# Kernel tuning notes

Measured on AMD Instinct MI355X. Metric: run time of the kernel, lower is better.

The kernel has to match this reference:

```python
import jax, jax.numpy as jnp
import numpy as np


def _grid_mesh(n):
    ys, xs = np.meshgrid(np.arange(n), np.arange(n), indexing='ij')
    verts = np.stack([xs, ys, np.zeros_like(xs)], -1).reshape(-1, 3).astype(np.float32) / (n - 1)
    idx = np.arange(n * n).reshape(n, n)
    v00 = idx[:-1, :-1].ravel(); v01 = idx[:-1, 1:].ravel()
    v10 = idx[1:, :-1].ravel(); v11 = idx[1:, 1:].ravel()
    faces = np.concatenate([np.stack([v00, v10, v01], 1), np.stack([v01, v10, v11], 1)], 0).astype(np.int32)
    e = np.concatenate([faces[:, [0, 1]], faces[:, [1, 2]], faces[:, [2, 0]]], 0)
    e = np.unique(np.sort(e, axis=1), axis=0).astype(np.int32)
    return verts, faces, e


def setup_inputs() -> dict:
    N_GRID, B, S = 200, 2, 5000
    verts_np, faces_np, edges_np = _grid_mesh(N_GRID)
    verts_np[:, 2] = 0.1 * np.sin(2 * np.pi * verts_np[:, 0]) * np.sin(2 * np.pi * verts_np[:, 1])
    key = jax.random.key(0)
    k1, k2, k3, k4 = jax.random.split(key, 4)
    verts_std = jnp.asarray(verts_np)
    verts_scr = verts_std[None] + 5e-4 * jax.random.normal(k1, (B,) + verts_std.shape, jnp.float32)
    xy = jax.random.uniform(k2, (B, S, 2), jnp.float32)
    z = 0.1 * jnp.sin(2 * jnp.pi * xy[..., 0]) * jnp.sin(2 * jnp.pi * xy[..., 1])
    trg_points = jnp.concatenate([xy, z[..., None]], -1)
    rand_face_u = jax.random.uniform(k3, (B, S), jnp.float32)
    rand_bary = jax.random.uniform(k4, (B, S, 2), jnp.float32)
    return {
        'verts_scr': verts_scr,
        'verts_std': verts_std,
        'trg_points': trg_points,
        'rand_face_u': rand_face_u,
        'rand_bary': rand_bary,
        'faces': jnp.asarray(faces_np),
        'edges': jnp.asarray(edges_np),
    }


def _cot_edges(verts, faces):
    # pytorch3d cot_laplacian: per-face cotangents, symmetrized edge list (6F entries).
    v0, v1, v2 = verts[faces[:, 0]], verts[faces[:, 1]], verts[faces[:, 2]]
    A = jnp.linalg.norm(v1 - v2, axis=1)
    B = jnp.linalg.norm(v0 - v2, axis=1)
    C = jnp.linalg.norm(v0 - v1, axis=1)
    A2, B2, C2 = A * A, B * B, C * C
    s = 0.5 * (A + B + C)
    area = jnp.sqrt(jnp.clip(s * (s - A) * (s - B) * (s - C), 1e-12, None))
    cot = jnp.stack([B2 + C2 - A2, A2 + C2 - B2, A2 + B2 - C2], axis=1) / (4.0 * area[:, None])
    ii = faces[:, jnp.array([1, 2, 0])].reshape(-1)
    jj = faces[:, jnp.array([2, 0, 1])].reshape(-1)
    src = jnp.concatenate([ii, jj])
    dst = jnp.concatenate([jj, ii])
    w = jnp.concatenate([cot.reshape(-1), cot.reshape(-1)])
    return src, dst, w


def _sample_points(verts, faces, u_face, r_bary):
    # area-weighted face sampling + pytorch3d barycentric coords
    v0, v1, v2 = verts[faces[:, 0]], verts[faces[:, 1]], verts[faces[:, 2]]
    areas = 0.5 * jnp.linalg.norm(jnp.cross(v1 - v0, v2 - v0), axis=1)
    cdf = jnp.cumsum(areas) / jnp.sum(areas)
    fidx = jnp.clip(jnp.searchsorted(cdf, u_face), 0, faces.shape[0] - 1)
    su = jnp.sqrt(r_bary[:, 0])
    w0, w1, w2 = 1.0 - su, su * (1.0 - r_bary[:, 1]), su * r_bary[:, 1]
    return w0[:, None] * v0[fidx] + w1[:, None] * v1[fidx] + w2[:, None] * v2[fidx]


def _chamfer(x, y):
    # squared-distance chamfer, mean over points then batch (pytorch3d defaults)
    d = (jnp.sum(x * x, -1)[:, :, None] + jnp.sum(y * y, -1)[:, None, :]
         - 2.0 * jnp.einsum('bsd,btd->bst', x, y))
    return jnp.min(d, 2).mean() + jnp.min(d, 1).mean()


def _forward(verts_scr, verts_std, trg_points, rand_face_u, rand_bary, faces, edges):
    Vn = verts_std.shape[0]
    # chamfer between sampled src surface points and target point cloud
    sample_scr = jax.vmap(lambda v, u, r: _sample_points(v, faces, u, r))(verts_scr, rand_face_u, rand_bary)
    loss_p0 = _chamfer(sample_scr, trg_points)
    loss_n1 = jnp.asarray(1e-5, verts_scr.dtype)  # tensor-target branch

    # cot laplacian smoothing (method='cot')
    def lap_one(v):
        src, dst, w = _cot_edges(v, faces)
        Lv = jax.ops.segment_sum(w[:, None] * v[dst], src, num_segments=Vn)
        rw = jax.ops.segment_sum(w, src, num_segments=Vn)
        inv = jnp.where(rw > 0, 1.0 / jnp.maximum(rw, 1e-12), 0.0)
        return jnp.linalg.norm(Lv * inv[:, None] - v, axis=1).mean()

    loss_lap = jax.vmap(lap_one)(verts_scr).mean()

    # edge loss against mean edge length of the std mesh
    target_len = jnp.linalg.norm(verts_std[edges[:, 0]] - verts_std[edges[:, 1]], axis=1).mean()
    elen = jnp.linalg.norm(verts_scr[:, edges[:, 0]] - verts_scr[:, edges[:, 1]], axis=-1)
    loss_edge = ((elen - target_len) ** 2).mean()

    # ARAP rigid loss on std-mesh cot connectivity/weights
    src, dst, w = _cot_edges(verts_std, faces)
    e_std = verts_std[src] - verts_std[dst]

    def rigid_one(v):
        e_scr = v[src] - v[dst]
        S = jax.ops.segment_sum(w[:, None, None] * e_std[:, :, None] * e_scr[:, None, :], src, num_segments=Vn)
        U, _, Vt = jnp.linalg.svd(S)
        R = jnp.matmul(jnp.swapaxes(Vt, -1, -2), jnp.swapaxes(U, -1, -2))
        flip = jnp.where(jnp.linalg.det(R) < 0, -1.0, 1.0)
        Vt2 = Vt.at[:, -1, :].multiply(flip[:, None])
        R = jnp.matmul(jnp.swapaxes(Vt2, -1, -2), jnp.swapaxes(U, -1, -2))
        res = e_scr - jnp.einsum('eij,ej->ei', R[src], e_std)
        return jax.ops.segment_sum(w * jnp.sum(res * res, 1), src, num_segments=Vn)

    loss_rigid = jax.vmap(rigid_one)(verts_scr).mean()
    return jnp.stack([loss_p0, loss_n1, loss_lap, loss_edge, loss_rigid])


def reference(verts_scr, verts_std, trg_points, rand_face_u, rand_bary, faces, edges):
    return _forward(verts_scr, verts_std, trg_points, rand_face_u, rand_bary, faces, edges)
```

## Files before the change

### kernel.cpp

```cpp
#include <hip/hip_runtime.h>
#include <math.h>

#define TPB 256
#define MAXDEG 8

static __device__ __forceinline__ void atomAddD(double* p, double v) {
  __hip_atomic_fetch_add(p, v, __ATOMIC_RELAXED, __HIP_MEMORY_SCOPE_AGENT);
}

static __device__ __forceinline__ double bredsum(double v) {
  __shared__ double sb[TPB];
  int t = threadIdx.x;
  sb[t] = v;
  __syncthreads();
  for (int o = TPB / 2; o > 0; o >>= 1) {
    if (t < o) sb[t] += sb[t + o];
    __syncthreads();
  }
  double r = sb[0];
  __syncthreads();
  return r;
}

template <int p, int q, int r>
static __device__ __forceinline__ void jrot(double A[3][3], double V[3][3]) {
  double apq = A[p][q];
  if (apq == 0.0) return;
  double app = A[p][p], aqq = A[q][q];
  double theta = (aqq - app) / (2.0 * apq);
  double t = 1.0 / (fabs(theta) + sqrt(theta * theta + 1.0));
  if (theta < 0.0) t = -t;
  double c = 1.0 / sqrt(t * t + 1.0), sn = t * c;
  A[p][p] = app - t * apq;
  A[q][q] = aqq + t * apq;
  A[p][q] = 0.0;
  A[q][p] = 0.0;
  double arp = A[r][p], arq = A[r][q];
  A[r][p] = c * arp - sn * arq; A[p][r] = A[r][p];
  A[r][q] = sn * arp + c * arq; A[q][r] = A[r][q];
#pragma unroll
  for (int k = 0; k < 3; k++) {
    double vkp = V[k][p], vkq = V[k][q];
    V[k][p] = c * vkp - sn * vkq;
    V[k][q] = sn * vkp + c * vkq;
  }
}

#define ESWAP(la, lax, lay, laz, lb, lbx, lby, lbz)                       \
  if (la < lb) {                                                          \
    double t_;                                                            \
    t_ = la; la = lb; lb = t_;                                            \
    t_ = lax; lax = lbx; lbx = t_;                                        \
    t_ = lay; lay = lby; lby = t_;                                        \
    t_ = laz; laz = lbz; lbz = t_;                                        \
  }

static __device__ void kabschR(const double S[3][3], double R9[9]) {
  double A[3][3];
#pragma unroll
  for (int a = 0; a < 3; a++)
#pragma unroll
    for (int c = 0; c < 3; c++)
      A[a][c] = S[0][a] * S[0][c] + S[1][a] * S[1][c] + S[2][a] * S[2][c];
  double V[3][3] = {{1, 0, 0}, {0, 1, 0}, {0, 0, 1}};
  for (int sw = 0; sw < 12; sw++) {
    double off = fabs(A[0][1]) + fabs(A[0][2]) + fabs(A[1][2]);
    double dia = fabs(A[0][0]) + fabs(A[1][1]) + fabs(A[2][2]);
    if (!(off > dia * 1e-15)) break;
    jrot<0, 1, 2>(A, V);
    jrot<0, 2, 1>(A, V);
    jrot<1, 2, 0>(A, V);
  }
  double l0 = A[0][0], l1 = A[1][1], l2 = A[2][2];
  double a0x = V[0][0], a0y = V[1][0], a0z = V[2][0];
  double a1x = V[0][1], a1y = V[1][1], a1z = V[2][1];
  double a2x = V[0][2], a2y = V[1][2], a2z = V[2][2];
  ESWAP(l0, a0x, a0y, a0z, l1, a1x, a1y, a1z);
  ESWAP(l0, a0x, a0y, a0z, l2, a2x, a2y, a2z);
  ESWAP(l1, a1x, a1y, a1z, l2, a2x, a2y, a2z);
  double R00 = 1, R01 = 0, R02 = 0, R10 = 0, R11 = 1, R12 = 0, R20 = 0, R21 = 0, R22 = 1;
  double b1x = S[0][0] * a0x + S[0][1] * a0y + S[0][2] * a0z;
  double b1y = S[1][0] * a0x + S[1][1] * a0y + S[1][2] * a0z;
  double b1z = S[2][0] * a0x + S[2][1] * a0y + S[2][2] * a0z;
  double b2x = S[0][0] * a1x + S[0][1] * a1y + S[0][2] * a1z;
  double b2y = S[1][0] * a1x + S[1][1] * a1y + S[1][2] * a1z;
  double b2z = S[2][0] * a1x + S[2][1] * a1y + S[2][2] * a1z;
  double n1 = sqrt(b1x * b1x + b1y * b1y + b1z * b1z);
  if (n1 > 1e-300 && isfinite(n1)) {
    double u1x = b1x / n1, u1y = b1y / n1, u1z = b1z / n1;
    double dp = u1x * b2x + u1y * b2y + u1z * b2z;
    b2x -= dp * u1x; b2y -= dp * u1y; b2z -= dp * u1z;
    double n2 = sqrt(b2x * b2x + b2y * b2y + b2z * b2z);
    double u2x, u2y, u2z;
    if (n2 > n1 * 1e-14) {
      u2x = b2x / n2; u2y = b2y / n2; u2z = b2z / n2;
    } else {
      double f0 = fabs(u1x), f1 = fabs(u1y), f2 = fabs(u1z);
      double e0, e1, e2;
      if (f0 <= f1 && f0 <= f2) { e0 = 1.0 - u1x * u1x; e1 = -u1x * u1y; e2 = -u1x * u1z; }
      else if (f1 <= f2)        { e0 = -u1y * u1x; e1 = 1.0 - u1y * u1y; e2 = -u1y * u1z; }
      else                      { e0 = -u1z * u1x; e1 = -u1z * u1y; e2 = 1.0 - u1z * u1z; }
      double nw = sqrt(e0 * e0 + e1 * e1 + e2 * e2);
      u2x = e0 / nw; u2y = e1 / nw; u2z = e2 / nw;
    }
    double u3x = u1y * u2z - u1z * u2y;
    double u3y = u1z * u2x - u1x * u2z;
    double u3z = u1x * u2y - u1y * u2x;
    double w3x = a0y * a1z - a0z * a1y;
    double w3y = a0z * a1x - a0x * a1z;
    double w3z = a0x * a1y - a0y * a1x;
    R00 = a0x * u1x + a1x * u2x + w3x * u3x;
    R01 = a0x * u1y + a1x * u2y + w3x * u3y;
    R02 = a0x * u1z + a1x * u2z + w3x * u3z;
    R10 = a0y * u1x + a1y * u2x + w3y * u3x;
    R11 = a0y * u1y + a1y * u2y + w3y * u3y;
    R12 = a0y * u1z + a1y * u2z + w3y * u3z;
    R20 = a0z * u1x + a1z * u2x + w3z * u3x;
    R21 = a0z * u1y + a1z * u2y + w3z * u3y;
    R22 = a0z * u1z + a1z * u2z + w3z * u3z;
  }
  R9[0] = R00; R9[1] = R01; R9[2] = R02;
  R9[3] = R10; R9[4] = R11; R9[5] = R12;
  R9[6] = R20; R9[7] = R21; R9[8] = R22;
}

static __device__ __forceinline__ void heronCots(double A2, double B2, double C2,
                                                 double* c0, double* c1, double* c2) {
  double A = sqrt(A2), Bl = sqrt(B2), C = sqrt(C2);
  double s = 0.5 * (A + Bl + C);
  double pr = s * (s - A) * (s - Bl) * (s - C);
  pr = pr < 1e-12 ? 1e-12 : pr;
  double inv4 = 1.0 / (4.0 * sqrt(pr));
  *c0 = (B2 + C2 - A2) * inv4;
  *c1 = (A2 + C2 - B2) * inv4;
  *c2 = (A2 + B2 - C2) * inv4;
}

__global__ void kPrep(const float* vscr, const float* vstd, const int* faces,
                      const int* edges, double* cdf, double* ccot, double* scot,
                      int* adjcnt, int4* adjtab, double* accEdgeStd,
                      int B, int Vn, int F, int E) {
  int i = blockIdx.x * TPB + threadIdx.x;
  if (i < B * F) {
    int b = i / F, f = i % F;
    const float* vb = vscr + (size_t)b * Vn * 3;
    int i0 = faces[f * 3], i1 = faces[f * 3 + 1], i2 = faces[f * 3 + 2];
    {
      double p0x = vb[i0 * 3], p0y = vb[i0 * 3 + 1], p0z = vb[i0 * 3 + 2];
      double p1x = vb[i1 * 3], p1y = vb[i1 * 3 + 1], p1z = vb[i1 * 3 + 2];
      double p2x = vb[i2 * 3], p2y = vb[i2 * 3 + 1], p2z = vb[i2 * 3 + 2];
      double ax = p1x - p0x, ay = p1y - p0y, az = p1z - p0z;
      double bx = p2x - p0x, by = p2y - p0y, bz = p2z - p0z;
      double cx = ay * bz - az * by, cy = az * bx - ax * bz, cz = ax * by - ay * bx;
      cdf[i] = 0.5 * sqrt(cx * cx + cy * cy + cz * cz);
      double dx = p1x - p2x, dy = p1y - p2y, dz = p1z - p2z;
      double A2 = dx * dx + dy * dy + dz * dz;
      double B2 = bx * bx + by * by + bz * bz;
      double C2 = ax * ax + ay * ay + az * az;
      double c0, c1, c2;
      heronCots(A2, B2, C2, &c0, &c1, &c2);
      ccot[(size_t)i * 3 + 0] = c0;
      ccot[(size_t)i * 3 + 1] = c1;
      ccot[(size_t)i * 3 + 2] = c2;
    }
    if (b == 0) {
      double p0x = vstd[i0 * 3], p0y = vstd[i0 * 3 + 1], p0z = vstd[i0 * 3 + 2];
      double p1x = vstd[i1 * 3], p1y = vstd[i1 * 3 + 1], p1z = vstd[i1 * 3 + 2];
      double p2x = vstd[i2 * 3], p2y = vstd[i2 * 3 + 1], p2z = vstd[i2 * 3 + 2];
      double ax = p1x - p0x, ay = p1y - p0y, az = p1z - p0z;
      double bx = p2x - p0x, by = p2y - p0y, bz = p2z - p0z;
      double dx = p1x - p2x, dy = p1y - p2y, dz = p1z - p2z;
      double A2 = dx * dx + dy * dy + dz * dz;
      double B2 = bx * bx + by * by + bz * bz;
      double C2 = ax * ax + ay * ay + az * az;
      double c0, c1, c2;
      heronCots(A2, B2, C2, &c0, &c1, &c2);
      scot[(size_t)f * 3 + 0] = c0;
      scot[(size_t)f * 3 + 1] = c1;
      scot[(size_t)f * 3 + 2] = c2;
      int f3 = f * 3;
      int s0 = atomicAdd(&adjcnt[i0], 1);
      if (s0 < MAXDEG) adjtab[(size_t)i0 * MAXDEG + s0] = make_int4(i1, i2, f3 + 1, f3 + 2);
      int s1 = atomicAdd(&adjcnt[i1], 1);
      if (s1 < MAXDEG) adjtab[(size_t)i1 * MAXDEG + s1] = make_int4(i2, i0, f3 + 2, f3 + 0);
      int s2 = atomicAdd(&adjcnt[i2], 1);
      if (s2 < MAXDEG) adjtab[(size_t)i2 * MAXDEG + s2] = make_int4(i0, i1, f3 + 0, f3 + 1);
    }
  }
  double eval = 0.0;
  if (i < E) {
    int e0 = edges[(size_t)i * 2], e1 = edges[(size_t)i * 2 + 1];
    double dx = (double)vstd[e0 * 3 + 0] - vstd[e1 * 3 + 0];
    double dy = (double)vstd[e0 * 3 + 1] - vstd[e1 * 3 + 1];
    double dz = (double)vstd[e0 * 3 + 2] - vstd[e1 * 3 + 2];
    eval = sqrt(dx * dx + dy * dy + dz * dz);
  }
  double r = bredsum(eval);
  if (threadIdx.x == 0) atomAddD(accEdgeStd, r);
}

__global__ void kScanFused(double* a, double* bsum, double* boffs, int F, int nc,
                           int B, int* cnt) {
  int blk = blockIdx.x;
  int b = blk / nc, c = blk % nc;
  int t = threadIdx.x, lane = t & 63, wid = t >> 6;
  int f = c * 1024 + t;
  size_t idx = (size_t)b * F + f;
  double v = (f < F) ? a[idx] : 0.0;
  double x = v;
#pragma unroll
  for (int o = 1; o < 64; o <<= 1) {
    double y = __shfl_up(x, o, 64);
    if (lane >= o) x += y;
  }
  __shared__ double wsum[16];
  __shared__ double woffs[16];
  if (lane == 63) wsum[wid] = x;
  __syncthreads();
  if (wid == 0) {
    double s = (lane < 16) ? wsum[lane] : 0.0;
    double xs = s;
#pragma unroll
    for (int o = 1; o < 16; o <<= 1) {
      double y = __shfl_up(xs, o, 64);
      if (lane >= o) xs += y;
    }
    double ex = __shfl_up(xs, 1, 64);
    if (lane < 16) woffs[lane] = (lane == 0) ? 0.0 : ex;
  }
  __syncthreads();
  x += woffs[wid];
  if (f < F) a[idx] = x;
  if (t == 1023) bsum[(size_t)b * nc + c] = x;
  __syncthreads();
  __shared__ int amlast;
  if (t == 0) {
    __threadfence();
    int old = __hip_atomic_fetch_add(cnt, 1, __ATOMIC_ACQ_REL, __HIP_MEMORY_SCOPE_AGENT);
    amlast = (old == (int)gridDim.x - 1) ? 1 : 0;
  }
  __syncthreads();
  if (amlast && wid == 0) {
    for (int bb = 0; bb < B; bb++) {
      double carry = 0.0;
      for (int base = 0; base < nc; base += 64) {
        int cc = base + lane;
        double s = (cc < nc) ? bsum[(size_t)bb * nc + cc] : 0.0;
        double xs = s;
#pragma unroll
        for (int o = 1; o < 64; o <<= 1) {
          double y = __shfl_up(xs, o, 64);
          if (lane >= o) xs += y;
        }
        double ex = __shfl_up(xs, 1, 64);
        double excl = (lane == 0) ? 0.0 : ex;
        if (cc < nc) boffs[(size_t)bb * nc + cc] = carry + excl;
        carry += __shfl(xs, 63, 64);
      }
    }
  }
}

__global__ void kSample(const float* verts, const int* faces, const double* cdf,
                        const double* bsum, const double* boffs,
                        const float* rfu, const float* rbary, float* samples,
                        int B, int Vn, int F, int S, int nc) {
  int i = blockIdx.x * blockDim.x + threadIdx.x;
  if (i >= B * S) return;
  int b = i / S;
  const double* bo = boffs + (size_t)b * nc;
  const double* bs = bsum + (size_t)b * nc;
  double total = bo[nc - 1] + bs[nc - 1];
  double tgt = (double)rfu[i] * total;
  int lo = 0, hi = nc;
  while (lo < hi) {
    int m = (lo + hi) >> 1;
    if (bo[m] + bs[m] < tgt) lo = m + 1; else hi = m;
  }
  int c = lo < nc ? lo : nc - 1;
  double thr = tgt - bo[c];
  const double* cc = cdf + (size_t)b * F + (size_t)c * 1024;
  int lim = F - c * 1024; if (lim > 1024) lim = 1024;
  lo = 0; hi = lim;
  while (lo < hi) {
    int m = (lo + hi) >> 1;
    if (cc[m] < thr) lo = m + 1; else hi = m;
  }
  int j = lo < lim ? lo : lim - 1;
  int f = c * 1024 + j;
  const float* vb = verts + (size_t)b * Vn * 3;
  int i0 = faces[f * 3], i1 = faces[f * 3 + 1], i2 = faces[f * 3 + 2];
  float r0 = rbary[(size_t)i * 2], r1 = rbary[(size_t)i * 2 + 1];
  float su = sqrtf(r0);
  float w0 = 1.f - su, w1 = su * (1.f - r1), w2 = su * r1;
  samples[(size_t)i * 3 + 0] = w0 * vb[i0 * 3 + 0] + w1 * vb[i1 * 3 + 0] + w2 * vb[i2 * 3 + 0];
  samples[(size_t)i * 3 + 1] = w0 * vb[i0 * 3 + 1] + w1 * vb[i1 * 3 + 1] + w2 * vb[i2 * 3 + 1];
  samples[(size_t)i * 3 + 2] = w0 * vb[i0 * 3 + 2] + w1 * vb[i1 * 3 + 2] + w2 * vb[i2 * 3 + 2];
}

__global__ void kChamferBoth(const float* smp, const float* trg, unsigned* rowmin,
                             int B, int S) {
  int z = blockIdx.z;
  int dir = z / B, b = z % B;
  const float* X = dir ? trg : smp;
  const float* Y = dir ? smp : trg;
  int i = blockIdx.x * TPB + threadIdx.x;
  int j0 = blockIdx.y * TPB;
  int n = min(TPB, S - j0);
  __shared__ float4 sy[TPB];
  const float* Yb = Y + ((size_t)b * S + j0) * 3;
  if ((int)threadIdx.x < n) {
    int t = threadIdx.x;
    sy[t] = make_float4(Yb[t * 3], Yb[t * 3 + 1], Yb[t * 3 + 2], 0.f);
  }
  __syncthreads();
  if (i >= S) return;
  const float* Xb = X + (size_t)b * S * 3;
  float x0 = Xb[i * 3], x1 = Xb[i * 3 + 1], x2 = Xb[i * 3 + 2];
  float inf = __int_as_float(0x7f800000);
  float m0 = inf, m1 = inf, m2 = inf, m3 = inf;
  int k = 0;
  for (; k + 4 <= n; k += 4) {
    float4 y0 = sy[k], y1 = sy[k + 1], y2 = sy[k + 2], y3 = sy[k + 3];
    float a0 = x0 - y0.x, b0 = x1 - y0.y, c0 = x2 - y0.z;
    float a1 = x0 - y1.x, b1 = x1 - y1.y, c1 = x2 - y1.z;
    float a2 = x0 - y2.x, b2 = x1 - y2.y, c2 = x2 - y2.z;
    float a3 = x0 - y3.x, b3 = x1 - y3.y, c3 = x2 - y3.z;
    m0 = fminf(m0, a0 * a0 + b0 * b0 + c0 * c0);
    m1 = fminf(m1, a1 * a1 + b1 * b1 + c1 * c1);
    m2 = fminf(m2, a2 * a2 + b2 * b2 + c2 * c2);
    m3 = fminf(m3, a3 * a3 + b3 * b3 + c3 * c3);
  }
  for (; k < n; k++) {
    float4 y = sy[k];
    float a = x0 - y.x, bb = x1 - y.y, cc = x2 - y.z;
    m0 = fminf(m0, a * a + bb * bb + cc * cc);
  }
  float mn = fminf(fminf(m0, m1), fminf(m2, m3));
  atomicMin(&rowmin[((size_t)dir * B + b) * S + i], __float_as_uint(mn));
}

__global__ void kMisc(const unsigned* rm, int nrm, const float* vscr, const int* edges,
                      int B, int Vn, int E, const double* tacc,
                      double* accCh, double* accEd) {
  int i = blockIdx.x * TPB + threadIdx.x;
  double v = 0.0;
  if (i < nrm) v = (double)__uint_as_float(rm[i]);
  double r = bredsum(v);
  if (threadIdx.x == 0) atomAddD(accCh, r);
  double tl = tacc[0] / (double)E;
  double val = 0.0;
  if (i < B * E) {
    int b = i / E, e = i % E;
    const float* vb = vscr + (size_t)b * Vn * 3;
    int e0 = edges[(size_t)e * 2], e1 = edges[(size_t)e * 2 + 1];
    double dx = (double)vb[e0 * 3 + 0] - vb[e1 * 3 + 0];
    double dy = (double)vb[e0 * 3 + 1] - vb[e1 * 3 + 1];
    double dz = (double)vb[e0 * 3 + 2] - vb[e1 * 3 + 2];
    double l = sqrt(dx * dx + dy * dy + dz * dz);
    double d = l - tl;
    val = d * d;
  }
  double r2 = bredsum(val);
  if (threadIdx.x == 0) atomAddD(accEd, r2);
}

__global__ void kVertexFin(const float* vstd, const float* vscr,
                           const int* cnt, const int4* adjtab, const double* scot,
                           const double* ccot, int B, int Vn, int F,
                           double* accum, int* done, float* out, int S, int E) {
  int idx = blockIdx.x * TPB + threadIdx.x;
  double vlap = 0.0, vrig = 0.0;
  if (idx < B * Vn) {
    int b = idx / Vn, v = idx % Vn;
    const float* cb = vscr + (size_t)b * Vn * 3;
    const double* ccb = ccot + (size_t)b * F * 3;
    double pasx = vstd[v * 3], pasy = vstd[v * 3 + 1], pasz = vstd[v * 3 + 2];
    double pacx = cb[v * 3], pacy = cb[v * 3 + 1], pacz = cb[v * 3 + 2];
    int n = cnt[v];
    if (n > MAXDEG) n = MAXDEG;
    const int4* at = adjtab + (size_t)v * MAXDEG;
    double S00 = 0, S01 = 0, S02 = 0, S10 = 0, S11 = 0, S12 = 0, S20 = 0, S21 = 0, S22 = 0;
    double Lx = 0, Ly = 0, Lz = 0, rw = 0, Qs = 0, Qc = 0;
    for (int k = 0; k < n; k++) {
      int4 e = at[k];
      int jb = e.x, jc = e.y;
      double cBs = scot[e.z], cCs = scot[e.w];
      double cBc = ccb[e.z], cCc = ccb[e.w];
      double pbsx = vstd[jb * 3], pbsy = vstd[jb * 3 + 1], pbsz = vstd[jb * 3 + 2];
      double pcsx = vstd[jc * 3], pcsy = vstd[jc * 3 + 1], pcsz = vstd[jc * 3 + 2];
      double pbcx = cb[jb * 3], pbcy = cb[jb * 3 + 1], pbcz = cb[jb * 3 + 2];
      double pccx = cb[jc * 3], pccy = cb[jc * 3 + 1], pccz = cb[jc * 3 + 2];
      Lx += cCc * pbcx + cBc * pccx;
      Ly += cCc * pbcy + cBc * pccy;
      Lz += cCc * pbcz + cBc * pccz;
      rw += cBc + cCc;
      double e1sx = pasx - pbsx, e1sy = pasy - pbsy, e1sz = pasz - pbsz;
      double e2sx = pasx - pcsx, e2sy = pasy - pcsy, e2sz = pasz - pcsz;
      double e1cx = pacx - pbcx, e1cy = pacy - pbcy, e1cz = pacz - pbcz;
      double e2cx = pacx - pccx, e2cy = pacy - pccy, e2cz = pacz - pccz;
      S00 += cCs * e1sx * e1cx + cBs * e2sx * e2cx;
      S01 += cCs * e1sx * e1cy + cBs * e2sx * e2cy;
      S02 += cCs * e1sx * e1cz + cBs * e2sx * e2cz;
      S10 += cCs * e1sy * e1cx + cBs * e2sy * e2cx;
      S11 += cCs * e1sy * e1cy + cBs * e2sy * e2cy;
      S12 += cCs * e1sy * e1cz + cBs * e2sy * e2cz;
      S20 += cCs * e1sz * e1cx + cBs * e2sz * e2cx;
      S21 += cCs * e1sz * e1cy + cBs * e2sz * e2cy;
      S22 += cCs * e1sz * e1cz + cBs * e2sz * e2cz;
      Qs += cCs * (e1sx * e1sx + e1sy * e1sy + e1sz * e1sz)
          + cBs * (e2sx * e2sx + e2sy * e2sy + e2sz * e2sz);
      Qc += cCs * (e1cx * e1cx + e1cy * e1cy + e1cz * e1cz)
          + cBs * (e2cx * e2cx + e2cy * e2cy + e2cz * e2cz);
    }
    double inv = (rw > 0.0) ? 1.0 / fmax(rw, 1e-12) : 0.0;
    double dx = Lx * inv - pacx, dy = Ly * inv - pacy, dz = Lz * inv - pacz;
    vlap = sqrt(dx * dx + dy * dy + dz * dz);
    double S[3][3] = {{S00, S01, S02}, {S10, S11, S12}, {S20, S21, S22}};
    double R9[9];
    kabschR(S, R9);
    double trRS = R9[0] * S00 + R9[1] * S10 + R9[2] * S20
                + R9[3] * S01 + R9[4] * S11 + R9[5] * S21
                + R9[6] * S02 + R9[7] * S12 + R9[8] * S22;
    vrig = Qc + Qs - 2.0 * trRS;
  }
  double r1 = bredsum(vlap);
  if (threadIdx.x == 0) atomAddD(accum + 1, r1);
  double r2 = bredsum(vrig);
  if (threadIdx.x == 0) atomAddD(accum + 4, r2);
  __shared__ int amlast;
  if (threadIdx.x == 0) {
    __threadfence();
    int old = __hip_atomic_fetch_add(done, 1, __ATOMIC_ACQ_REL, __HIP_MEMORY_SCOPE_AGENT);
    amlast = (old == (int)gridDim.x - 1) ? 1 : 0;
  }
  __syncthreads();
  if (amlast && threadIdx.x == 0) {
    double a0 = __hip_atomic_load(accum + 0, __ATOMIC_RELAXED, __HIP_MEMORY_SCOPE_AGENT);
    double a1 = __hip_atomic_load(accum + 1, __ATOMIC_RELAXED, __HIP_MEMORY_SCOPE_AGENT);
    double a3 = __hip_atomic_load(accum + 3, __ATOMIC_RELAXED, __HIP_MEMORY_SCOPE_AGENT);
    double a4 = __hip_atomic_load(accum + 4, __ATOMIC_RELAXED, __HIP_MEMORY_SCOPE_AGENT);
    out[0] = (float)(a0 / ((double)B * S));
    out[1] = 1e-5f;
    out[2] = (float)(a1 / ((double)B * Vn));
    out[3] = (float)(a3 / ((double)B * E));
    out[4] = (float)(a4 / ((double)B * Vn));
  }
}

extern "C" void kernel_launch(void* const* d_in, const int* in_sizes, int n_in,
                              void* d_out, int out_size, void* d_ws, size_t ws_size,
                              hipStream_t stream) {
  const float* vscr = (const float*)d_in[0];
  const float* vstd = (const float*)d_in[1];
  const float* trg  = (const float*)d_in[2];
  const float* rfu  = (const float*)d_in[3];
  const float* rby  = (const float*)d_in[4];
  const int* faces  = (const int*)d_in[5];
  const int* edges  = (const int*)d_in[6];
  float* out = (float*)d_out;

  int nVs = in_sizes[1];
  int Vn = nVs / 3;
  int B = in_sizes[0] / nVs;
  int S = in_sizes[3] / B;
  int F = in_sizes[5] / 3;
  int E = in_sizes[6] / 2;
  int nc = (F + 1023) / 1024;

  char* p = (char*)d_ws;
  auto alloc = [&](size_t bytes) -> void* {
    void* r = (void*)p;
    p += (bytes + 255) & ~(size_t)255;
    return r;
  };
  double* cdf   = (double*)alloc((size_t)B * F * sizeof(double));
  double* bsum  = (double*)alloc((size_t)B * nc * sizeof(double));
  double* boffs = (double*)alloc((size_t)B * nc * sizeof(double));
  double* scot  = (double*)alloc((size_t)F * 3 * sizeof(double));
  double* ccot  = (double*)alloc((size_t)B * F * 3 * sizeof(double));
  float* samples   = (float*)alloc((size_t)B * S * 3 * sizeof(float));
  unsigned* rowmin = (unsigned*)alloc((size_t)2 * B * S * sizeof(unsigned));
  int4* adjtab  = (int4*)alloc((size_t)Vn * MAXDEG * sizeof(int4));
  size_t zbytes = (size_t)Vn * sizeof(int) + 8 * sizeof(int) + 8 * sizeof(double);
  char* zbase   = (char*)alloc(zbytes);
  int* adjcnt   = (int*)zbase;
  int* cnts     = (int*)(zbase + (size_t)Vn * sizeof(int));
  double* accum = (double*)(zbase + (size_t)Vn * sizeof(int) + 8 * sizeof(int));

  hipMemsetAsync(zbase, 0, zbytes, stream);
  int nrm = 2 * B * S;
  hipMemsetAsync(rowmin, 0xFF, (size_t)nrm * sizeof(unsigned), stream);

  int BF = B * F;
  kPrep<<<(BF + TPB - 1) / TPB, TPB, 0, stream>>>(vscr, vstd, faces, edges, cdf, ccot,
                                                  scot, adjcnt, adjtab, accum + 2,
                                                  B, Vn, F, E);
  kScanFused<<<B * nc, 1024, 0, stream>>>(cdf, bsum, boffs, F, nc, B, cnts + 0);
  kSample<<<(B * S + TPB - 1) / TPB, TPB, 0, stream>>>(vscr, faces, cdf, bsum, boffs,
                                                       rfu, rby, samples, B, Vn, F, S, nc);
  dim3 cg((S + TPB - 1) / TPB, (S + TPB - 1) / TPB, 2 * B);
  kChamferBoth<<<cg, TPB, 0, stream>>>(samples, trg, rowmin, B, S);
  int nmisc = nrm > B * E ? nrm : B * E;
  kMisc<<<(nmisc + TPB - 1) / TPB, TPB, 0, stream>>>(rowmin, nrm, vscr, edges, B, Vn, E,
                                                     accum + 2, accum + 0, accum + 3);
  kVertexFin<<<(B * Vn + TPB - 1) / TPB, TPB, 0, stream>>>(vstd, vscr, adjcnt, adjtab,
                                                           scot, ccot, B, Vn, F,
                                                           accum, cnts + 1, out, S, E);
}
```

Baseline: 197.4 us.

## Fuse misc reductions into vertex kernel, double chamfer rows per thread, cap Jacobi sweeps

Removes the separate kMisc launch by folding the chamfer row-min sum and edge-length loss into kVertexFin, whose grid is enlarged to cover all three index ranges. The chamfer kernel now processes two query points per thread, so each shared-memory load of a target point is reused twice and half as many blocks are launched. The Jacobi eigen-solver sweep cap drops from 12 to 8. Edge threads in the fused kernel far outnumber vertex threads, so many blocks do light work alongside the heavy Kabsch blocks, and the lower sweep cap could cut convergence short for hard matrices.

```diff
diff --git a/kernel.cpp b/kernel.cpp
--- a/kernel.cpp
+++ b/kernel.cpp
@@ -63,7 +63,7 @@
     for (int c = 0; c < 3; c++)
       A[a][c] = S[0][a] * S[0][c] + S[1][a] * S[1][c] + S[2][a] * S[2][c];
   double V[3][3] = {{1, 0, 0}, {0, 1, 0}, {0, 0, 1}};
-  for (int sw = 0; sw < 12; sw++) {
+  for (int sw = 0; sw < 8; sw++) {
     double off = fabs(A[0][1]) + fabs(A[0][2]) + fabs(A[1][2]);
     double dia = fabs(A[0][0]) + fabs(A[1][1]) + fabs(A[2][2]);
     if (!(off > dia * 1e-15)) break;
@@ -304,7 +304,8 @@
   int dir = z / B, b = z % B;
   const float* X = dir ? trg : smp;
   const float* Y = dir ? smp : trg;
-  int i = blockIdx.x * TPB + threadIdx.x;
+  int ia = blockIdx.x * (TPB * 2) + threadIdx.x;
+  int ib = ia + TPB;
   int j0 = blockIdx.y * TPB;
   int n = min(TPB, S - j0);
   __shared__ float4 sy[TPB];
@@ -314,44 +315,47 @@
     sy[t] = make_float4(Yb[t * 3], Yb[t * 3 + 1], Yb[t * 3 + 2], 0.f);
   }
   __syncthreads();
-  if (i >= S) return;
   const float* Xb = X + (size_t)b * S * 3;
-  float x0 = Xb[i * 3], x1 = Xb[i * 3 + 1], x2 = Xb[i * 3 + 2];
+  bool aok = ia < S, bok = ib < S;
+  float ax = 0, ay = 0, az = 0, bx = 0, by = 0, bz = 0;
+  if (aok) { ax = Xb[ia * 3]; ay = Xb[ia * 3 + 1]; az = Xb[ia * 3 + 2]; }
+  if (bok) { bx = Xb[ib * 3]; by = Xb[ib * 3 + 1]; bz = Xb[ib * 3 + 2]; }
   float inf = __int_as_float(0x7f800000);
-  float m0 = inf, m1 = inf, m2 = inf, m3 = inf;
+  float ma0 = inf, ma1 = inf, mb0 = inf, mb1 = inf;
   int k = 0;
-  for (; k + 4 <= n; k += 4) {
-    float4 y0 = sy[k], y1 = sy[k + 1], y2 = sy[k + 2], y3 = sy[k + 3];
-    float a0 = x0 - y0.x, b0 = x1 - y0.y, c0 = x2 - y0.z;
-    float a1 = x0 - y1.x, b1 = x1 - y1.y, c1 = x2 - y1.z;
-    float a2 = x0 - y2.x, b2 = x1 - y2.y, c2 = x2 - y2.z;
-    float a3 = x0 - y3.x, b3 = x1 - y3.y, c3 = x2 - y3.z;
-    m0 = fminf(m0, a0 * a0 + b0 * b0 + c0 * c0);
-    m1 = fminf(m1, a1 * a1 + b1 * b1 + c1 * c1);
-    m2 = fminf(m2, a2 * a2 + b2 * b2 + c2 * c2);
-    m3 = fminf(m3, a3 * a3 + b3 * b3 + c3 * c3);
+  for (; k + 2 <= n; k += 2) {
+    float4 y0 = sy[k], y1 = sy[k + 1];
+    float a0 = ax - y0.x, a1 = ay - y0.y, a2 = az - y0.z;
+    float a3 = ax - y1.x, a4 = ay - y1.y, a5 = az - y1.z;
+    float b0 = bx - y0.x, b1 = by - y0.y, b2 = bz - y0.z;
+    float b3 = bx - y1.x, b4 = by - y1.y, b5 = bz - y1.z;
+    ma0 = fminf(ma0, a0 * a0 + a1 * a1 + a2 * a2);
+    ma1 = fminf(ma1, a3 * a3 + a4 * a4 + a5 * a5);
+    mb0 = fminf(mb0, b0 * b0 + b1 * b1 + b2 * b2);
+    mb1 = fminf(mb1, b3 * b3 + b4 * b4 + b5 * b5);
   }
   for (; k < n; k++) {
     float4 y = sy[k];
-    float a = x0 - y.x, bb = x1 - y.y, cc = x2 - y.z;
-    m0 = fminf(m0, a * a + bb * bb + cc * cc);
-  }
-  float mn = fminf(fminf(m0, m1), fminf(m2, m3));
-  atomicMin(&rowmin[((size_t)dir * B + b) * S + i], __float_as_uint(mn));
-}
-
-__global__ void kMisc(const unsigned* rm, int nrm, const float* vscr, const int* edges,
-                      int B, int Vn, int E, const double* tacc,
-                      double* accCh, double* accEd) {
-  int i = blockIdx.x * TPB + threadIdx.x;
-  double v = 0.0;
-  if (i < nrm) v = (double)__uint_as_float(rm[i]);
-  double r = bredsum(v);
-  if (threadIdx.x == 0) atomAddD(accCh, r);
-  double tl = tacc[0] / (double)E;
-  double val = 0.0;
-  if (i < B * E) {
-    int b = i / E, e = i % E;
+    float a0 = ax - y.x, a1 = ay - y.y, a2 = az - y.z;
+    float b0 = bx - y.x, b1 = by - y.y, b2 = bz - y.z;
+    ma0 = fminf(ma0, a0 * a0 + a1 * a1 + a2 * a2);
+    mb0 = fminf(mb0, b0 * b0 + b1 * b1 + b2 * b2);
+  }
+  size_t base = ((size_t)dir * B + b) * S;
+  if (aok) atomicMin(&rowmin[base + ia], __float_as_uint(fminf(ma0, ma1)));
+  if (bok) atomicMin(&rowmin[base + ib], __float_as_uint(fminf(mb0, mb1)));
+}
+
+__global__ void kVertexFin(const float* vstd, const float* vscr,
+                           const int* cnt, const int4* adjtab, const double* scot,
+                           const double* ccot, const unsigned* rm, int nrm,
+                           const int* edges, int B, int Vn, int F, int E,
+                           double* accum, int* done, float* out, int S) {
+  int idx = blockIdx.x * TPB + threadIdx.x;
+  double tl = accum[2] / (double)E;
+  double vedge = 0.0;
+  if (idx < B * E) {
+    int b = idx / E, e = idx % E;
     const float* vb = vscr + (size_t)b * Vn * 3;
     int e0 = edges[(size_t)e * 2], e1 = edges[(size_t)e * 2 + 1];
     double dx = (double)vb[e0 * 3 + 0] - vb[e1 * 3 + 0];
@@ -359,17 +363,10 @@
     double dz = (double)vb[e0 * 3 + 2] - vb[e1 * 3 + 2];
     double l = sqrt(dx * dx + dy * dy + dz * dz);
     double d = l - tl;
-    val = d * d;
-  }
-  double r2 = bredsum(val);
-  if (threadIdx.x == 0) atomAddD(accEd, r2);
-}
-
-__global__ void kVertexFin(const float* vstd, const float* vscr,
-                           const int* cnt, const int4* adjtab, const double* scot,
-                           const double* ccot, int B, int Vn, int F,
-                           double* accum, int* done, float* out, int S, int E) {
-  int idx = blockIdx.x * TPB + threadIdx.x;
+    vedge = d * d;
+  }
+  double vch = 0.0;
+  if (idx < nrm) vch = (double)__uint_as_float(rm[idx]);
   double vlap = 0.0, vrig = 0.0;
   if (idx < B * Vn) {
     int b = idx / Vn, v = idx % Vn;
@@ -424,10 +421,15 @@
                 + R9[6] * S02 + R9[7] * S12 + R9[8] * S22;
     vrig = Qc + Qs - 2.0 * trRS;
   }
-  double r1 = bredsum(vlap);
-  if (threadIdx.x == 0) atomAddD(accum + 1, r1);
-  double r2 = bredsum(vrig);
-  if (threadIdx.x == 0) atomAddD(accum + 4, r2);
+  double r;
+  r = bredsum(vedge);
+  if (threadIdx.x == 0) atomAddD(accum + 3, r);
+  r = bredsum(vch);
+  if (threadIdx.x == 0) atomAddD(accum + 0, r);
+  r = bredsum(vlap);
+  if (threadIdx.x == 0) atomAddD(accum + 1, r);
+  r = bredsum(vrig);
+  if (threadIdx.x == 0) atomAddD(accum + 4, r);
   __shared__ int amlast;
   if (threadIdx.x == 0) {
     __threadfence();
@@ -499,12 +501,13 @@
   kScanFused<<<B * nc, 1024, 0, stream>>>(cdf, bsum, boffs, F, nc, B, cnts + 0);
   kSample<<<(B * S + TPB - 1) / TPB, TPB, 0, stream>>>(vscr, faces, cdf, bsum, boffs,
                                                        rfu, rby, samples, B, Vn, F, S, nc);
-  dim3 cg((S + TPB - 1) / TPB, (S + TPB - 1) / TPB, 2 * B);
+  dim3 cg((S + TPB * 2 - 1) / (TPB * 2), (S + TPB - 1) / TPB, 2 * B);
   kChamferBoth<<<cg, TPB, 0, stream>>>(samples, trg, rowmin, B, S);
-  int nmisc = nrm > B * E ? nrm : B * E;
-  kMisc<<<(nmisc + TPB - 1) / TPB, TPB, 0, stream>>>(rowmin, nrm, vscr, edges, B, Vn, E,
-                                                     accum + 2, accum + 0, accum + 3);
-  kVertexFin<<<(B * Vn + TPB - 1) / TPB, TPB, 0, stream>>>(vstd, vscr, adjcnt, adjtab,
-                                                           scot, ccot, B, Vn, F,
-                                                           accum, cnts + 1, out, S, E);
-}
+  int nfin = B * E;
+  if (nfin < B * Vn) nfin = B * Vn;
+  if (nfin < nrm) nfin = nrm;
+  kVertexFin<<<(nfin + TPB - 1) / TPB, TPB, 0, stream>>>(vstd, vscr, adjcnt, adjtab,
+                                                         scot, ccot, rowmin, nrm, edges,
+                                                         B, Vn, F, E, accum, cnts + 1,
+                                                         out, S);
+}
```

Result: slower. 209.8 us (+6.3%).

## Split vertex finalize into 8-lane neighbor gather and separate Kabsch kernel

Applied to the files above, without the earlier changes.

The per-vertex loop over up to eight adjacency entries is spread across eight lanes, one neighbor each, and reduced with shuffles, so the gather loads run in parallel instead of serially per thread. The 3x3 covariance and the Q terms are written to a workspace buffer, and a second kernel runs the Jacobi-based Kabsch rotation one vertex per thread. The Jacobi sweep cap also drops from 12 to 8. This adds a kernel launch and a global round-trip of eleven doubles per vertex, and the lower sweep cap could cost accuracy on poorly conditioned matrices.

```diff
diff --git a/kernel.cpp b/kernel.cpp
--- a/kernel.cpp
+++ b/kernel.cpp
@@ -63,7 +63,7 @@
     for (int c = 0; c < 3; c++)
       A[a][c] = S[0][a] * S[0][c] + S[1][a] * S[1][c] + S[2][a] * S[2][c];
   double V[3][3] = {{1, 0, 0}, {0, 1, 0}, {0, 0, 1}};
-  for (int sw = 0; sw < 12; sw++) {
+  for (int sw = 0; sw < 8; sw++) {
     double off = fabs(A[0][1]) + fabs(A[0][2]) + fabs(A[1][2]);
     double dia = fabs(A[0][0]) + fabs(A[1][1]) + fabs(A[2][2]);
     if (!(off > dia * 1e-15)) break;
@@ -365,69 +365,107 @@
   if (threadIdx.x == 0) atomAddD(accEd, r2);
 }
 
-__global__ void kVertexFin(const float* vstd, const float* vscr,
-                           const int* cnt, const int4* adjtab, const double* scot,
-                           const double* ccot, int B, int Vn, int F,
-                           double* accum, int* done, float* out, int S, int E) {
-  int idx = blockIdx.x * TPB + threadIdx.x;
-  double vlap = 0.0, vrig = 0.0;
-  if (idx < B * Vn) {
-    int b = idx / Vn, v = idx % Vn;
+#define RED8(x) { x += __shfl_xor(x, 1, 8); x += __shfl_xor(x, 2, 8); x += __shfl_xor(x, 4, 8); }
+__global__ void kGather(const float* vstd, const float* vscr,
+                        const int* cnt, const int4* adjtab, const double* scot,
+                        const double* ccot, double* Sbuf, int B, int Vn, int F,
+                        double* accLap) {
+  int t = blockIdx.x * TPB + threadIdx.x;
+  int g = t >> 3, sub = t & 7;
+  int NG = B * Vn;
+  double vlap = 0.0;
+  if (g < NG) {
+    int b = g / Vn, v = g % Vn;
     const float* cb = vscr + (size_t)b * Vn * 3;
     const double* ccb = ccot + (size_t)b * F * 3;
     double pasx = vstd[v * 3], pasy = vstd[v * 3 + 1], pasz = vstd[v * 3 + 2];
     double pacx = cb[v * 3], pacy = cb[v * 3 + 1], pacz = cb[v * 3 + 2];
     int n = cnt[v];
     if (n > MAXDEG) n = MAXDEG;
-    const int4* at = adjtab + (size_t)v * MAXDEG;
-    double S00 = 0, S01 = 0, S02 = 0, S10 = 0, S11 = 0, S12 = 0, S20 = 0, S21 = 0, S22 = 0;
-    double Lx = 0, Ly = 0, Lz = 0, rw = 0, Qs = 0, Qc = 0;
-    for (int k = 0; k < n; k++) {
-      int4 e = at[k];
-      int jb = e.x, jc = e.y;
-      double cBs = scot[e.z], cCs = scot[e.w];
-      double cBc = ccb[e.z], cCc = ccb[e.w];
-      double pbsx = vstd[jb * 3], pbsy = vstd[jb * 3 + 1], pbsz = vstd[jb * 3 + 2];
-      double pcsx = vstd[jc * 3], pcsy = vstd[jc * 3 + 1], pcsz = vstd[jc * 3 + 2];
-      double pbcx = cb[jb * 3], pbcy = cb[jb * 3 + 1], pbcz = cb[jb * 3 + 2];
-      double pccx = cb[jc * 3], pccy = cb[jc * 3 + 1], pccz = cb[jc * 3 + 2];
-      Lx += cCc * pbcx + cBc * pccx;
-      Ly += cCc * pbcy + cBc * pccy;
-      Lz += cCc * pbcz + cBc * pccz;
-      rw += cBc + cCc;
-      double e1sx = pasx - pbsx, e1sy = pasy - pbsy, e1sz = pasz - pbsz;
-      double e2sx = pasx - pcsx, e2sy = pasy - pcsy, e2sz = pasz - pcsz;
-      double e1cx = pacx - pbcx, e1cy = pacy - pbcy, e1cz = pacz - pbcz;
-      double e2cx = pacx - pccx, e2cy = pacy - pccy, e2cz = pacz - pccz;
-      S00 += cCs * e1sx * e1cx + cBs * e2sx * e2cx;
-      S01 += cCs * e1sx * e1cy + cBs * e2sx * e2cy;
-      S02 += cCs * e1sx * e1cz + cBs * e2sx * e2cz;
-      S10 += cCs * e1sy * e1cx + cBs * e2sy * e2cx;
-      S11 += cCs * e1sy * e1cy + cBs * e2sy * e2cy;
-      S12 += cCs * e1sy * e1cz + cBs * e2sy * e2cz;
-      S20 += cCs * e1sz * e1cx + cBs * e2sz * e2cx;
-      S21 += cCs * e1sz * e1cy + cBs * e2sz * e2cy;
-      S22 += cCs * e1sz * e1cz + cBs * e2sz * e2cz;
-      Qs += cCs * (e1sx * e1sx + e1sy * e1sy + e1sz * e1sz)
-          + cBs * (e2sx * e2sx + e2sy * e2sy + e2sz * e2sz);
-      Qc += cCs * (e1cx * e1cx + e1cy * e1cy + e1cz * e1cz)
-          + cBs * (e2cx * e2cx + e2cy * e2cy + e2cz * e2cz);
+    int slot = sub < n ? sub : n - 1;
+    double m = (sub < n) ? 1.0 : 0.0;
+    int4 e = adjtab[(size_t)v * MAXDEG + slot];
+    int jb = e.x, jc = e.y;
+    double cBs = m * scot[e.z], cCs = m * scot[e.w];
+    double cBc = m * ccb[e.z], cCc = m * ccb[e.w];
+    double pbsx = vstd[jb * 3], pbsy = vstd[jb * 3 + 1], pbsz = vstd[jb * 3 + 2];
+    double pcsx = vstd[jc * 3], pcsy = vstd[jc * 3 + 1], pcsz = vstd[jc * 3 + 2];
+    double pbcx = cb[jb * 3], pbcy = cb[jb * 3 + 1], pbcz = cb[jb * 3 + 2];
+    double pccx = cb[jc * 3], pccy = cb[jc * 3 + 1], pccz = cb[jc * 3 + 2];
+    double Lx = cCc * pbcx + cBc * pccx;
+    double Ly = cCc * pbcy + cBc * pccy;
+    double Lz = cCc * pbcz + cBc * pccz;
+    double rw = cBc + cCc;
+    double e1sx = pasx - pbsx, e1sy = pasy - pbsy, e1sz = pasz - pbsz;
+    double e2sx = pasx - pcsx, e2sy = pasy - pcsy, e2sz = pasz - pcsz;
+    double e1cx = pacx - pbcx, e1cy = pacy - pbcy, e1cz = pacz - pbcz;
+    double e2cx = pacx - pccx, e2cy = pacy - pccy, e2cz = pacz - pccz;
+    double S00 = cCs * e1sx * e1cx + cBs * e2sx * e2cx;
+    double S01 = cCs * e1sx * e1cy + cBs * e2sx * e2cy;
+    double S02 = cCs * e1sx * e1cz + cBs * e2sx * e2cz;
+    double S10 = cCs * e1sy * e1cx + cBs * e2sy * e2cx;
+    double S11 = cCs * e1sy * e1cy + cBs * e2sy * e2cy;
+    double S12 = cCs * e1sy * e1cz + cBs * e2sy * e2cz;
+    double S20 = cCs * e1sz * e1cx + cBs * e2sz * e2cx;
+    double S21 = cCs * e1sz * e1cy + cBs * e2sz * e2cy;
+    double S22 = cCs * e1sz * e1cz + cBs * e2sz * e2cz;
+    double Qs = cCs * (e1sx * e1sx + e1sy * e1sy + e1sz * e1sz)
+              + cBs * (e2sx * e2sx + e2sy * e2sy + e2sz * e2sz);
+    double Qc = cCs * (e1cx * e1cx + e1cy * e1cy + e1cz * e1cz)
+              + cBs * (e2cx * e2cx + e2cy * e2cy + e2cz * e2cz);
+    RED8(S00) RED8(S01) RED8(S02)
+    RED8(S10) RED8(S11) RED8(S12)
+    RED8(S20) RED8(S21) RED8(S22)
+    RED8(Lx) RED8(Ly) RED8(Lz)
+    RED8(rw) RED8(Qs) RED8(Qc)
+    if (sub == 0) {
+      double inv = (rw > 0.0) ? 1.0 / fmax(rw, 1e-12) : 0.0;
+      double dx = Lx * inv - pacx, dy = Ly * inv - pacy, dz = Lz * inv - pacz;
+      vlap = sqrt(dx * dx + dy * dy + dz * dz);
+      Sbuf[(size_t)0 * NG + g] = S00;
+      Sbuf[(size_t)1 * NG + g] = S01;
+      Sbuf[(size_t)2 * NG + g] = S02;
+      Sbuf[(size_t)3 * NG + g] = S10;
+      Sbuf[(size_t)4 * NG + g] = S11;
+      Sbuf[(size_t)5 * NG + g] = S12;
+      Sbuf[(size_t)6 * NG + g] = S20;
+      Sbuf[(size_t)7 * NG + g] = S21;
+      Sbuf[(size_t)8 * NG + g] = S22;
+      Sbuf[(size_t)9 * NG + g] = Qs;
+      Sbuf[(size_t)10 * NG + g] = Qc;
     }
-    double inv = (rw > 0.0) ? 1.0 / fmax(rw, 1e-12) : 0.0;
-    double dx = Lx * inv - pacx, dy = Ly * inv - pacy, dz = Lz * inv - pacz;
-    vlap = sqrt(dx * dx + dy * dy + dz * dz);
-    double S[3][3] = {{S00, S01, S02}, {S10, S11, S12}, {S20, S21, S22}};
+  }
+  double r = bredsum(vlap);
+  if (threadIdx.x == 0) atomAddD(accLap, r);
+}
+
+__global__ void kKabschFin(const double* Sbuf, int B, int Vn,
+                           double* accum, int* done, float* out, int S, int E) {
+  int idx = blockIdx.x * TPB + threadIdx.x;
+  int NG = B * Vn;
+  double vrig = 0.0;
+  if (idx < NG) {
+    double S00 = Sbuf[(size_t)0 * NG + idx];
+    double S01 = Sbuf[(size_t)1 * NG + idx];
+    double S02 = Sbuf[(size_t)2 * NG + idx];
+    double S10 = Sbuf[(size_t)3 * NG + idx];
+    double S11 = Sbuf[(size_t)4 * NG + idx];
+    double S12 = Sbuf[(size_t)5 * NG + idx];
+    double S20 = Sbuf[(size_t)6 * NG + idx];
+    double S21 = Sbuf[(size_t)7 * NG + idx];
+    double S22 = Sbuf[(size_t)8 * NG + idx];
+    double Qs = Sbuf[(size_t)9 * NG + idx];
+    double Qc = Sbuf[(size_t)10 * NG + idx];
+    double Smat[3][3] = {{S00, S01, S02}, {S10, S11, S12}, {S20, S21, S22}};
     double R9[9];
-    kabschR(S, R9);
+    kabschR(Smat, R9);
     double trRS = R9[0] * S00 + R9[1] * S10 + R9[2] * S20
                 + R9[3] * S01 + R9[4] * S11 + R9[5] * S21
                 + R9[6] * S02 + R9[7] * S12 + R9[8] * S22;
     vrig = Qc + Qs - 2.0 * trRS;
   }
-  double r1 = bredsum(vlap);
-  if (threadIdx.x == 0) atomAddD(accum + 1, r1);
-  double r2 = bredsum(vrig);
-  if (threadIdx.x == 0) atomAddD(accum + 4, r2);
+  double r = bredsum(vrig);
+  if (threadIdx.x == 0) atomAddD(accum + 4, r);
   __shared__ int amlast;
   if (threadIdx.x == 0) {
     __threadfence();
@@ -479,6 +517,7 @@
   double* boffs = (double*)alloc((size_t)B * nc * sizeof(double));
   double* scot  = (double*)alloc((size_t)F * 3 * sizeof(double));
   double* ccot  = (double*)alloc((size_t)B * F * 3 * sizeof(double));
+  double* Sbuf  = (double*)alloc((size_t)11 * B * Vn * sizeof(double));
   float* samples   = (float*)alloc((size_t)B * S * 3 * sizeof(float));
   unsigned* rowmin = (unsigned*)alloc((size_t)2 * B * S * sizeof(unsigned));
   int4* adjtab  = (int4*)alloc((size_t)Vn * MAXDEG * sizeof(int4));
@@ -504,7 +543,10 @@
   int nmisc = nrm > B * E ? nrm : B * E;
   kMisc<<<(nmisc + TPB - 1) / TPB, TPB, 0, stream>>>(rowmin, nrm, vscr, edges, B, Vn, E,
                                                      accum + 2, accum + 0, accum + 3);
-  kVertexFin<<<(B * Vn + TPB - 1) / TPB, TPB, 0, stream>>>(vstd, vscr, adjcnt, adjtab,
-                                                           scot, ccot, B, Vn, F,
-                                                           accum, cnts + 1, out, S, E);
-}
+  int ngt = B * Vn * 8;
+  kGather<<<(ngt + TPB - 1) / TPB, TPB, 0, stream>>>(vstd, vscr, adjcnt, adjtab,
+                                                     scot, ccot, Sbuf, B, Vn, F,
+                                                     accum + 1);
+  kKabschFin<<<(B * Vn + TPB - 1) / TPB, TPB, 0, stream>>>(Sbuf, B, Vn, accum,
+                                                           cnts + 1, out, S, E);
+}
```

Result: slower. 229.2 us (+16.1%).

## Split per-vertex ARAP accumulation across four lanes and fold rowmin init into prep

Applied to the files above, without the earlier changes.

The vertex finalization kernel now gives each vertex four threads. Each thread handles up to two adjacency slots, and the partial sums are combined with width-4 shuffles, so the serial neighbor loop gets more parallelism. The rowmin initialization memset is replaced by writes inside kPrep, which removes a separate memset operation. The Jacobi sweep cap in the Kabsch solve drops from 12 to 8, which may reduce accuracy for slowly converging matrices. Having only one lane in four run the SVD leaves lanes idle, and the vertex kernel now launches four times as many threads.

```diff
diff --git a/kernel.cpp b/kernel.cpp
--- a/kernel.cpp
+++ b/kernel.cpp
@@ -63,7 +63,7 @@
     for (int c = 0; c < 3; c++)
       A[a][c] = S[0][a] * S[0][c] + S[1][a] * S[1][c] + S[2][a] * S[2][c];
   double V[3][3] = {{1, 0, 0}, {0, 1, 0}, {0, 0, 1}};
-  for (int sw = 0; sw < 12; sw++) {
+  for (int sw = 0; sw < 8; sw++) {
     double off = fabs(A[0][1]) + fabs(A[0][2]) + fabs(A[1][2]);
     double dia = fabs(A[0][0]) + fabs(A[1][1]) + fabs(A[2][2]);
     if (!(off > dia * 1e-15)) break;
@@ -139,8 +139,9 @@
 __global__ void kPrep(const float* vscr, const float* vstd, const int* faces,
                       const int* edges, double* cdf, double* ccot, double* scot,
                       int* adjcnt, int4* adjtab, double* accEdgeStd,
-                      int B, int Vn, int F, int E) {
+                      unsigned* rowmin, int nrm, int B, int Vn, int F, int E) {
   int i = blockIdx.x * TPB + threadIdx.x;
+  if (i < nrm) rowmin[i] = 0xFFFFFFFFu;
   if (i < B * F) {
     int b = i / F, f = i % F;
     const float* vb = vscr + (size_t)b * Vn * 3;
@@ -365,28 +366,33 @@
   if (threadIdx.x == 0) atomAddD(accEd, r2);
 }
 
+#define RED4(x) { x += __shfl_xor(x, 1, 4); x += __shfl_xor(x, 2, 4); }
 __global__ void kVertexFin(const float* vstd, const float* vscr,
                            const int* cnt, const int4* adjtab, const double* scot,
                            const double* ccot, int B, int Vn, int F,
                            double* accum, int* done, float* out, int S, int E) {
-  int idx = blockIdx.x * TPB + threadIdx.x;
+  int t = blockIdx.x * TPB + threadIdx.x;
+  int g = t >> 2, sub = t & 3;
   double vlap = 0.0, vrig = 0.0;
-  if (idx < B * Vn) {
-    int b = idx / Vn, v = idx % Vn;
+  if (g < B * Vn) {
+    int b = g / Vn, v = g % Vn;
     const float* cb = vscr + (size_t)b * Vn * 3;
     const double* ccb = ccot + (size_t)b * F * 3;
     double pasx = vstd[v * 3], pasy = vstd[v * 3 + 1], pasz = vstd[v * 3 + 2];
     double pacx = cb[v * 3], pacy = cb[v * 3 + 1], pacz = cb[v * 3 + 2];
     int n = cnt[v];
     if (n > MAXDEG) n = MAXDEG;
-    const int4* at = adjtab + (size_t)v * MAXDEG;
     double S00 = 0, S01 = 0, S02 = 0, S10 = 0, S11 = 0, S12 = 0, S20 = 0, S21 = 0, S22 = 0;
     double Lx = 0, Ly = 0, Lz = 0, rw = 0, Qs = 0, Qc = 0;
-    for (int k = 0; k < n; k++) {
-      int4 e = at[k];
+#pragma unroll
+    for (int k = 0; k < 2; k++) {
+      int slot = sub + 4 * k;
+      int sl = slot < n ? slot : n - 1;
+      double m = (slot < n) ? 1.0 : 0.0;
+      int4 e = adjtab[(size_t)v * MAXDEG + sl];
       int jb = e.x, jc = e.y;
-      double cBs = scot[e.z], cCs = scot[e.w];
-      double cBc = ccb[e.z], cCc = ccb[e.w];
+      double cBs = m * scot[e.z], cCs = m * scot[e.w];
+      double cBc = m * ccb[e.z], cCc = m * ccb[e.w];
       double pbsx = vstd[jb * 3], pbsy = vstd[jb * 3 + 1], pbsz = vstd[jb * 3 + 2];
       double pcsx = vstd[jc * 3], pcsy = vstd[jc * 3 + 1], pcsz = vstd[jc * 3 + 2];
       double pbcx = cb[jb * 3], pbcy = cb[jb * 3 + 1], pbcz = cb[jb * 3 + 2];
@@ -413,16 +419,23 @@
       Qc += cCs * (e1cx * e1cx + e1cy * e1cy + e1cz * e1cz)
           + cBs * (e2cx * e2cx + e2cy * e2cy + e2cz * e2cz);
     }
-    double inv = (rw > 0.0) ? 1.0 / fmax(rw, 1e-12) : 0.0;
-    double dx = Lx * inv - pacx, dy = Ly * inv - pacy, dz = Lz * inv - pacz;
-    vlap = sqrt(dx * dx + dy * dy + dz * dz);
-    double S[3][3] = {{S00, S01, S02}, {S10, S11, S12}, {S20, S21, S22}};
-    double R9[9];
-    kabschR(S, R9);
-    double trRS = R9[0] * S00 + R9[1] * S10 + R9[2] * S20
-                + R9[3] * S01 + R9[4] * S11 + R9[5] * S21
-                + R9[6] * S02 + R9[7] * S12 + R9[8] * S22;
-    vrig = Qc + Qs - 2.0 * trRS;
+    RED4(S00) RED4(S01) RED4(S02)
+    RED4(S10) RED4(S11) RED4(S12)
+    RED4(S20) RED4(S21) RED4(S22)
+    RED4(Lx) RED4(Ly) RED4(Lz)
+    RED4(rw) RED4(Qs) RED4(Qc)
+    if (sub == 0) {
+      double inv = (rw > 0.0) ? 1.0 / fmax(rw, 1e-12) : 0.0;
+      double dx = Lx * inv - pacx, dy = Ly * inv - pacy, dz = Lz * inv - pacz;
+      vlap = sqrt(dx * dx + dy * dy + dz * dz);
+      double Smat[3][3] = {{S00, S01, S02}, {S10, S11, S12}, {S20, S21, S22}};
+      double R9[9];
+      kabschR(Smat, R9);
+      double trRS = R9[0] * S00 + R9[1] * S10 + R9[2] * S20
+                  + R9[3] * S01 + R9[4] * S11 + R9[5] * S21
+                  + R9[6] * S02 + R9[7] * S12 + R9[8] * S22;
+      vrig = Qc + Qs - 2.0 * trRS;
+    }
   }
   double r1 = bredsum(vlap);
   if (threadIdx.x == 0) atomAddD(accum + 1, r1);
@@ -490,12 +503,11 @@
 
   hipMemsetAsync(zbase, 0, zbytes, stream);
   int nrm = 2 * B * S;
-  hipMemsetAsync(rowmin, 0xFF, (size_t)nrm * sizeof(unsigned), stream);
 
   int BF = B * F;
   kPrep<<<(BF + TPB - 1) / TPB, TPB, 0, stream>>>(vscr, vstd, faces, edges, cdf, ccot,
                                                   scot, adjcnt, adjtab, accum + 2,
-                                                  B, Vn, F, E);
+                                                  rowmin, nrm, B, Vn, F, E);
   kScanFused<<<B * nc, 1024, 0, stream>>>(cdf, bsum, boffs, F, nc, B, cnts + 0);
   kSample<<<(B * S + TPB - 1) / TPB, TPB, 0, stream>>>(vscr, faces, cdf, bsum, boffs,
                                                        rfu, rby, samples, B, Vn, F, S, nc);
@@ -504,7 +516,8 @@
   int nmisc = nrm > B * E ? nrm : B * E;
   kMisc<<<(nmisc + TPB - 1) / TPB, TPB, 0, stream>>>(rowmin, nrm, vscr, edges, B, Vn, E,
                                                      accum + 2, accum + 0, accum + 3);
-  kVertexFin<<<(B * Vn + TPB - 1) / TPB, TPB, 0, stream>>>(vstd, vscr, adjcnt, adjtab,
-                                                           scot, ccot, B, Vn, F,
-                                                           accum, cnts + 1, out, S, E);
-}
+  int nvt = B * Vn * 4;
+  kVertexFin<<<(nvt + TPB - 1) / TPB, TPB, 0, stream>>>(vstd, vscr, adjcnt, adjtab,
+                                                        scot, ccot, B, Vn, F,
+                                                        accum, cnts + 1, out, S, E);
+}
```

Result: slower. 230.0 us (+16.5%).
